# Kernel optimization log

Measured on AMD Instinct MI355X. Metric: run time of the kernel, lower is better.

The kernel has to match this reference:

```python
import jax, jax.numpy as jnp
import numpy as np
from jax import lax

NUM_GROUP = 512
GROUP_SIZE = 32


def fps(xyz, npoint):
    """Farthest point sampling. xyz: [B, N, 3] -> centers [B, npoint, 3]."""
    B, N, _ = xyz.shape
    big = jnp.asarray(1e10, xyz.dtype)

    def body(carry, _):
        min_d, farthest = carry  # [B, N], [B]
        centroid = jnp.take_along_axis(xyz, farthest[:, None, None], axis=1)  # [B,1,3]
        d = jnp.sum((xyz - centroid) ** 2, axis=-1)  # [B, N]
        min_d = jnp.minimum(min_d, d)
        nxt = jnp.argmax(min_d, axis=-1).astype(jnp.int32)
        return (min_d, nxt), farthest

    init = (jnp.full((B, N), big, xyz.dtype), jnp.zeros((B,), jnp.int32))
    _, idxs = lax.scan(body, init, None, length=npoint)  # [npoint, B]
    idxs = idxs.T  # [B, npoint]
    return jnp.take_along_axis(xyz, idxs[..., None], axis=1)  # [B, npoint, 3]


def knn_idx(xyz, center, k):
    """xyz [B,N,3], center [B,G,3] -> idx [B,G,k] of k nearest (squared L2)."""
    # [B, G, N] squared distances
    d2 = jnp.sum((center[:, :, None, :] - xyz[:, None, :, :]) ** 2, axis=-1)
    _, idx = lax.top_k(-d2, k)  # smallest distances
    return idx


def setup_inputs() -> dict:
    key = jax.random.key(0)
    xyz = jax.random.normal(key, (32, 3, 8192), dtype=jnp.float32)
    return {"xyz": xyz}


def reference(xyz):
    # xyz: [B, 3, N] -> [B, N, 3]
    pts = jnp.transpose(xyz, (0, 2, 1))[:, :, :3]
    B, N, _ = pts.shape
    center = fps(pts, NUM_GROUP)                  # [B, G, 3]
    idx = knn_idx(pts, center, GROUP_SIZE)        # [B, G, k]
    flat_idx = idx.reshape(B, NUM_GROUP * GROUP_SIZE)
    neighborhood = jnp.take_along_axis(pts, flat_idx[..., None], axis=1)
    neighborhood = neighborhood.reshape(B, NUM_GROUP, GROUP_SIZE, 3)
    neighborhood = neighborhood - center[:, :, None, :]
    return neighborhood, center
```

## Files before the change

### kernel.cpp

```cpp
#include <hip/hip_runtime.h>

typedef unsigned long long u64;
typedef unsigned int u32;
typedef float v2f __attribute__((ext_vector_type(2)));

#define BATCH 32
#define NPTS  8192
#define NGRP  512
#define KNN_K 32

#define FPS_T 256
#define FPS_W (FPS_T / 64)
#define PPAIR (NPTS / FPS_T / 2)

#define KNN_WPB 8
#define KNN_T   (KNN_WPB * 64)
#define QCAP    128

#define NCH     (NPTS / 64)
#define GC      16
#define NCELL   (GC * GC * GC)
#define QB      512
#define CBT     256
#define WSF     (4 * NPTS + NCH * 6)

__device__ __forceinline__ float sq3(float dx, float dy, float dz) {
    return __fadd_rn(__fadd_rn(__fmul_rn(dx, dx), __fmul_rn(dy, dy)), __fmul_rn(dz, dz));
}

__device__ __forceinline__ u64 packdi(float d, int n) {
    return ((u64)__float_as_uint(d) << 32) | (u32)n;
}

__device__ __forceinline__ u64 umin64(u64 a, u64 b) { return a < b ? a : b; }
__device__ __forceinline__ u64 umax64(u64 a, u64 b) { return a > b ? a : b; }

__device__ __forceinline__ u64 shfl_xor_u64(u64 v, int m) {
    int lo = __shfl_xor((int)(u32)v, m, 64);
    int hi = __shfl_xor((int)(u32)(v >> 32), m, 64);
    return ((u64)(u32)hi << 32) | (u32)lo;
}

__device__ __forceinline__ u64 shfl_u64(u64 v, int src) {
    int lo = __shfl((int)(u32)v, src, 64);
    int hi = __shfl((int)(u32)(v >> 32), src, 64);
    return ((u64)(u32)hi << 32) | (u32)lo;
}

template <int CTRL>
__device__ __forceinline__ u64 dpp_max_step(u64 k) {
    u32 plo = (u32)__builtin_amdgcn_update_dpp(0, (int)(u32)k, CTRL, 0xF, 0xF, true);
    u32 phi = (u32)__builtin_amdgcn_update_dpp(0, (int)(u32)(k >> 32), CTRL, 0xF, 0xF, true);
    u64 p = ((u64)phi << 32) | plo;
    return k > p ? k : p;
}
__device__ __forceinline__ u64 dpp_wave_max(u64 k) {
    k = dpp_max_step<0x111>(k);
    k = dpp_max_step<0x112>(k);
    k = dpp_max_step<0x114>(k);
    k = dpp_max_step<0x118>(k);
    k = dpp_max_step<0x142>(k);
    k = dpp_max_step<0x143>(k);
    return k;
}

__device__ __forceinline__ u64 lane_sort64(u64 v, int lane) {
#pragma unroll
    for (int k = 2; k <= 64; k <<= 1) {
#pragma unroll
        for (int j = k >> 1; j > 0; j >>= 1) {
            u64 p = shfl_xor_u64(v, j);
            bool keepmin = (((lane & k) == 0) == ((lane & j) == 0));
            u64 mn = umin64(v, p), mx = umax64(v, p);
            v = keepmin ? mn : mx;
        }
    }
    return v;
}

__device__ __forceinline__ u64 lane_merge64(u64 m, u64 c, int lane) {
    u64 cr = shfl_xor_u64(c, 63);
    u64 z = umin64(m, cr);
#pragma unroll
    for (int dd = 32; dd > 0; dd >>= 1) {
        u64 p = shfl_xor_u64(z, dd);
        u64 mn = umin64(z, p), mx = umax64(z, p);
        z = (lane & dd) ? mx : mn;
    }
    return z;
}

__device__ __forceinline__ void knn_step(u64& m, u64& tau, int& cnt, u64* sbuf,
                                         float x, float y, float z,
                                         float cx, float cy, float cz,
                                         int n, int lane) {
    float d = sq3(__fsub_rn(x, cx), __fsub_rn(y, cy), __fsub_rn(z, cz));
    u64 kk = packdi(d, n);
    bool cand = kk < tau;
    u64 mask = __ballot(cand);
    if (mask) {
        u32 below = __builtin_amdgcn_mbcnt_hi(
            (u32)(mask >> 32), __builtin_amdgcn_mbcnt_lo((u32)mask, 0));
        if (cand) sbuf[cnt + below] = kk;
        cnt += (int)__popcll(mask);
        if (cnt >= 64) {
            u64 c = sbuf[lane];
            c = lane_sort64(c, lane);
            m = lane_merge64(m, c, lane);
            tau = shfl_u64(m, 31);
            int rem = cnt - 64;
            if (lane < rem) sbuf[lane] = sbuf[64 + lane];
            cnt = rem;
        }
    }
}

__device__ __forceinline__ int qbin(float v) {
    int c = (int)((v + 4.0f) * 64.0f);
    c = c < 0 ? 0 : c;
    return c > (QB - 1) ? (QB - 1) : c;
}
__device__ __forceinline__ u32 part3_4(u32 v) {
    return (v & 1u) | ((v & 2u) << 2) | ((v & 4u) << 4) | ((v & 8u) << 6);
}

struct FpsLds {
    float sx[NPTS]; float sy[NPTS]; float sz[NPTS];
    u64 s_key[2][FPS_W];
    float s_out[NGRP * 3];
};
struct BldLds {
    u32 hist[NCELL];
    u32 hq[3][QB];
    float sxl[NPTS]; float syl[NPTS]; float szl[NPTS];
    u32 wtot[3][CBT / 64];
};

__global__ __launch_bounds__(CBT) void fps_build_kernel(const float* __restrict__ in,
                                                        float* __restrict__ ws,
                                                        float* __restrict__ centers) {
#pragma clang fp contract(off)
    __shared__ alignas(16) char smem[sizeof(BldLds)];

    const int t = threadIdx.x;
    const int lane = t & 63;
    const int w = t >> 6;

    if (blockIdx.x < BATCH) {
        FpsLds& S = *reinterpret_cast<FpsLds*>(smem);
        const int b = blockIdx.x;
        const float* xp = in + (size_t)b * 3 * NPTS;
        const float* yp = xp + NPTS;
        const float* zp = xp + 2 * NPTS;

        v2f xr[PPAIR], yr[PPAIR], zr[PPAIR], md[PPAIR];
#pragma unroll
        for (int i = 0; i < PPAIR; ++i) {
            int n = i * (2 * FPS_T) + 2 * t;
            xr[i] = *(const v2f*)(xp + n);
            yr[i] = *(const v2f*)(yp + n);
            zr[i] = *(const v2f*)(zp + n);
            *(v2f*)(S.sx + n) = xr[i];
            *(v2f*)(S.sy + n) = yr[i];
            *(v2f*)(S.sz + n) = zr[i];
            md[i] = (v2f){1e10f, 1e10f};
        }
        __syncthreads();

        int cur = 0;
        for (int r = 0; r < NGRP; ++r) {
            const float cx = S.sx[cur], cy = S.sy[cur], cz = S.sz[cur];
            if (t == 0) {
                S.s_out[r * 3 + 0] = cx;
                S.s_out[r * 3 + 1] = cy;
                S.s_out[r * 3 + 2] = cz;
            }

            float bd0 = -1.0f, bd1 = -1.0f;
            int   bi0 = 0,     bi1 = 0;
#pragma unroll
            for (int i = 0; i < PPAIR; ++i) {
                v2f dx = xr[i] - cx;
                v2f dy = yr[i] - cy;
                v2f dz = zr[i] - cz;
                v2f dd = dx * dx + dy * dy + dz * dz;
                md[i] = __builtin_elementwise_min(md[i], dd);
                int n = i * (2 * FPS_T) + 2 * t;
                if (md[i].x > bd0) { bd0 = md[i].x; bi0 = n; }
                if (md[i].y > bd1) { bd1 = md[i].y; bi1 = n + 1; }
            }
            u64 k0 = ((u64)__float_as_uint(bd0) << 32) | (u32)(~(u32)bi0);
            u64 k1 = ((u64)__float_as_uint(bd1) << 32) | (u32)(~(u32)bi1);
            u64 k = dpp_wave_max(umax64(k0, k1));
            if ((t & 63) == 63) S.s_key[r & 1][w] = k;
            __syncthreads();
            u64 m = umax64(umax64(S.s_key[r & 1][0], S.s_key[r & 1][1]),
                           umax64(S.s_key[r & 1][2], S.s_key[r & 1][3]));
            cur = (int)(~(u32)m);
        }

        __syncthreads();
        float* cdst = centers + (size_t)b * NGRP * 3;
        for (int i = t; i < NGRP * 3; i += FPS_T) cdst[i] = S.s_out[i];
        return;
    }

    BldLds& S = *reinterpret_cast<BldLds*>(smem);
    const int b = blockIdx.x - BATCH;
    const float* xp = in + (size_t)b * 3 * NPTS;
    const float* yp = xp + NPTS;
    const float* zp = xp + 2 * NPTS;
    float* wsb = ws + (size_t)b * WSF;
    float* ws_sx = wsb;
    float* ws_sy = wsb + NPTS;
    float* ws_sz = wsb + 2 * NPTS;
    u32*   ws_si = (u32*)(wsb + 3 * NPTS);
    float* ws_ab = wsb + 4 * NPTS;

    for (int i = t; i < NCELL; i += CBT) S.hist[i] = 0;
    for (int i = t; i < 3 * QB; i += CBT) (&S.hq[0][0])[i] = 0;
    __syncthreads();

    for (int i = t; i < NPTS; i += CBT) {
        atomicAdd(&S.hq[0][qbin(xp[i])], 1u);
        atomicAdd(&S.hq[1][qbin(yp[i])], 1u);
        atomicAdd(&S.hq[2][qbin(zp[i])], 1u);
    }
    __syncthreads();

    {
        u32 va0 = S.hq[0][2 * t], vb0 = S.hq[0][2 * t + 1];
        u32 va1 = S.hq[1][2 * t], vb1 = S.hq[1][2 * t + 1];
        u32 va2 = S.hq[2][2 * t], vb2 = S.hq[2][2 * t + 1];
        u32 s0 = va0 + vb0, s1 = va1 + vb1, s2 = va2 + vb2;
        u32 x0 = s0, x1 = s1, x2 = s2;
#pragma unroll
        for (int d = 1; d < 64; d <<= 1) {
            u32 y0 = __shfl_up(x0, d, 64), y1 = __shfl_up(x1, d, 64), y2 = __shfl_up(x2, d, 64);
            if (lane >= d) { x0 += y0; x1 += y1; x2 += y2; }
        }
        if (lane == 63) { S.wtot[0][w] = x0; S.wtot[1][w] = x1; S.wtot[2][w] = x2; }
        __syncthreads();
        u32 b0 = 0, b1 = 0, b2 = 0;
        for (int j = 0; j < w; ++j) { b0 += S.wtot[0][j]; b1 += S.wtot[1][j]; b2 += S.wtot[2][j]; }
        u32 e0 = b0 + x0 - s0, e1 = b1 + x1 - s1, e2 = b2 + x2 - s2;
        S.hq[0][2 * t] = e0 >> 9;  S.hq[0][2 * t + 1] = (e0 + va0) >> 9;
        S.hq[1][2 * t] = e1 >> 9;  S.hq[1][2 * t + 1] = (e1 + va1) >> 9;
        S.hq[2][2 * t] = e2 >> 9;  S.hq[2][2 * t + 1] = (e2 + va2) >> 9;
    }
    __syncthreads();

    for (int i = t; i < NPTS; i += CBT) {
        int pc = (int)(part3_4(S.hq[0][qbin(xp[i])]) |
                       (part3_4(S.hq[1][qbin(yp[i])]) << 1) |
                       (part3_4(S.hq[2][qbin(zp[i])]) << 2));
        atomicAdd(&S.hist[pc], 1u);
    }
    __syncthreads();

    {
        u32 h[NCELL / CBT];
        u32 lsum = 0;
#pragma unroll
        for (int j = 0; j < NCELL / CBT; ++j) { h[j] = S.hist[t * (NCELL / CBT) + j]; lsum += h[j]; }
        u32 x = lsum;
#pragma unroll
        for (int d = 1; d < 64; d <<= 1) {
            u32 y = __shfl_up(x, d, 64);
            if (lane >= d) x += y;
        }
        if (lane == 63) S.wtot[0][w] = x;
        __syncthreads();
        u32 base = 0;
        for (int j = 0; j < w; ++j) base += S.wtot[0][j];
        u32 run = base + x - lsum;
#pragma unroll
        for (int j = 0; j < NCELL / CBT; ++j) {
            u32 c = h[j];
            S.hist[t * (NCELL / CBT) + j] = run;
            run += c;
        }
    }
    __syncthreads();

    for (int i = t; i < NPTS; i += CBT) {
        float X = xp[i], Y = yp[i], Z = zp[i];
        int pc = (int)(part3_4(S.hq[0][qbin(X)]) |
                       (part3_4(S.hq[1][qbin(Y)]) << 1) |
                       (part3_4(S.hq[2][qbin(Z)]) << 2));
        u32 pos = atomicAdd(&S.hist[pc], 1u);
        S.sxl[pos] = X; S.syl[pos] = Y; S.szl[pos] = Z;
        ws_si[pos] = (u32)i;
    }
    __syncthreads();

    for (int i = t; i < NPTS; i += CBT) {
        ws_sx[i] = S.sxl[i]; ws_sy[i] = S.syl[i]; ws_sz[i] = S.szl[i];
    }
    for (int q = w; q < NCH; q += CBT / 64) {
        int p = q * 64 + lane;
        float X = S.sxl[p], Y = S.syl[p], Z = S.szl[p];
        float xlo = X, xhi = X, ylo = Y, yhi = Y, zlo = Z, zhi = Z;
#pragma unroll
        for (int d = 1; d < 64; d <<= 1) {
            xlo = fminf(xlo, __shfl_xor(xlo, d, 64)); xhi = fmaxf(xhi, __shfl_xor(xhi, d, 64));
            ylo = fminf(ylo, __shfl_xor(ylo, d, 64)); yhi = fmaxf(yhi, __shfl_xor(yhi, d, 64));
            zlo = fminf(zlo, __shfl_xor(zlo, d, 64)); zhi = fmaxf(zhi, __shfl_xor(zhi, d, 64));
        }
        if (lane == 0) {
            float* a = ws_ab + q * 6;
            a[0] = xlo; a[1] = xhi; a[2] = ylo; a[3] = yhi; a[4] = zlo; a[5] = zhi;
        }
    }
}

__global__ __launch_bounds__(KNN_T) void knn_kernel(const float* __restrict__ in,
                                                    const float* __restrict__ centers,
                                                    const float* __restrict__ ws,
                                                    float* __restrict__ out) {
    __shared__ float s_ab[NCH * 6];
    __shared__ u64 sbuf[KNN_WPB][QCAP];

    const int wave = threadIdx.x >> 6;
    const int lane = threadIdx.x & 63;
    const int cid  = blockIdx.x * KNN_WPB + wave;
    const int b    = cid >> 9;

    const float* xp = in + (size_t)b * 3 * NPTS;
    const float* yp = xp + NPTS;
    const float* zp = xp + 2 * NPTS;
    const float* wsb = ws + (size_t)b * WSF;
    const float* sxs = wsb;
    const float* sys = wsb + NPTS;
    const float* szs = wsb + 2 * NPTS;
    const u32*   sidx = (const u32*)(wsb + 3 * NPTS);
    const float* ab = wsb + 4 * NPTS;

    for (int i = threadIdx.x; i < NCH * 6; i += KNN_T) s_ab[i] = ab[i];
    __syncthreads();

    const float cx = centers[cid * 3 + 0];
    const float cy = centers[cid * 3 + 1];
    const float cz = centers[cid * 3 + 2];

    u64 k0, k1;
    {
        const float* a0 = &s_ab[lane * 6];
        float dx = fmaxf(fmaxf(__fsub_rn(a0[0], cx), __fsub_rn(cx, a0[1])), 0.0f);
        float dy = fmaxf(fmaxf(__fsub_rn(a0[2], cy), __fsub_rn(cy, a0[3])), 0.0f);
        float dz = fmaxf(fmaxf(__fsub_rn(a0[4], cz), __fsub_rn(cz, a0[5])), 0.0f);
        k0 = ((u64)__float_as_uint(dx * dx + dy * dy + dz * dz) << 32) | (u32)lane;
        const float* a1 = &s_ab[(lane + 64) * 6];
        dx = fmaxf(fmaxf(__fsub_rn(a1[0], cx), __fsub_rn(cx, a1[1])), 0.0f);
        dy = fmaxf(fmaxf(__fsub_rn(a1[2], cy), __fsub_rn(cy, a1[3])), 0.0f);
        dz = fmaxf(fmaxf(__fsub_rn(a1[4], cz), __fsub_rn(cz, a1[5])), 0.0f);
        k1 = ((u64)__float_as_uint(dx * dx + dy * dy + dz * dz) << 32) | (u32)(lane + 64);
    }

    u64 m, tau;
    int cnt = 0;

    {
        u64 inv = dpp_wave_max(~umin64(k0, k1));
        u64 got = ~shfl_u64(inv, 63);
        int c = (int)(u32)got;
        int p = c * 64 + lane;
        float X = sxs[p], Y = sys[p], Z = szs[p];
        int n = (int)sidx[p];
        m = lane_sort64(packdi(sq3(__fsub_rn(X, cx), __fsub_rn(Y, cy), __fsub_rn(Z, cz)), n),
                        lane);
        tau = shfl_u64(m, 31);
        if (lane == (c & 63)) { if (c < 64) k0 = ~0ull; else k1 = ~0ull; }
    }

    for (int it = 1; it < NCH; ++it) {
        u64 inv = dpp_wave_max(~umin64(k0, k1));
        u64 got = ~shfl_u64(inv, 63);
        float lb = __uint_as_float((u32)(got >> 32));
        float tau_d = __uint_as_float((u32)(tau >> 32));
        if (lb * 0.999f > tau_d) break;
        int c = (int)(u32)got;
        int p = c * 64 + lane;
        float X = sxs[p], Y = sys[p], Z = szs[p];
        int n = (int)sidx[p];
        knn_step(m, tau, cnt, sbuf[wave], X, Y, Z, cx, cy, cz, n, lane);
        if (lane == (c & 63)) { if (c < 64) k0 = ~0ull; else k1 = ~0ull; }
    }

    while (cnt > 0) {
        int take = cnt < 64 ? cnt : 64;
        u64 v = sbuf[wave][lane];
        u64 c = (lane < take) ? v : ~0ull;
        c = lane_sort64(c, lane);
        m = lane_merge64(m, c, lane);
        int rem = cnt - take;
        if (lane < rem) sbuf[wave][lane] = sbuf[wave][64 + lane];
        cnt = rem;
    }

    if (lane < KNN_K) {
        int n = (int)(u32)m;
        size_t o = (size_t)cid * (KNN_K * 3) + (size_t)lane * 3;
        out[o + 0] = __fsub_rn(xp[n], cx);
        out[o + 1] = __fsub_rn(yp[n], cy);
        out[o + 2] = __fsub_rn(zp[n], cz);
    }
}

__global__ __launch_bounds__(FPS_T) void fps_kernel(const float* __restrict__ in,
                                                    float* __restrict__ centers) {
#pragma clang fp contract(off)
    __shared__ float sx[NPTS];
    __shared__ float sy[NPTS];
    __shared__ float sz[NPTS];
    __shared__ u64 s_key[2][FPS_W];
    __shared__ float s_out[NGRP * 3];

    const int b = blockIdx.x;
    const int t = threadIdx.x;
    const int w = t >> 6;
    const float* xp = in + (size_t)b * 3 * NPTS;
    const float* yp = xp + NPTS;
    const float* zp = xp + 2 * NPTS;

    v2f xr[PPAIR], yr[PPAIR], zr[PPAIR], md[PPAIR];
#pragma unroll
    for (int i = 0; i < PPAIR; ++i) {
        int n = i * (2 * FPS_T) + 2 * t;
        xr[i] = *(const v2f*)(xp + n);
        yr[i] = *(const v2f*)(yp + n);
        zr[i] = *(const v2f*)(zp + n);
        *(v2f*)(sx + n) = xr[i];
        *(v2f*)(sy + n) = yr[i];
        *(v2f*)(sz + n) = zr[i];
        md[i] = (v2f){1e10f, 1e10f};
    }
    __syncthreads();

    int cur = 0;
    for (int r = 0; r < NGRP; ++r) {
        const float cx = sx[cur], cy = sy[cur], cz = sz[cur];
        if (t == 0) {
            s_out[r * 3 + 0] = cx;
            s_out[r * 3 + 1] = cy;
            s_out[r * 3 + 2] = cz;
        }
        float bd0 = -1.0f, bd1 = -1.0f;
        int   bi0 = 0,     bi1 = 0;
#pragma unroll
        for (int i = 0; i < PPAIR; ++i) {
            v2f dx = xr[i] - cx;
            v2f dy = yr[i] - cy;
            v2f dz = zr[i] - cz;
            v2f dd = dx * dx + dy * dy + dz * dz;
            md[i] = __builtin_elementwise_min(md[i], dd);
            int n = i * (2 * FPS_T) + 2 * t;
            if (md[i].x > bd0) { bd0 = md[i].x; bi0 = n; }
            if (md[i].y > bd1) { bd1 = md[i].y; bi1 = n + 1; }
        }
        u64 k0 = ((u64)__float_as_uint(bd0) << 32) | (u32)(~(u32)bi0);
        u64 k1 = ((u64)__float_as_uint(bd1) << 32) | (u32)(~(u32)bi1);
        u64 k = dpp_wave_max(umax64(k0, k1));
        if ((t & 63) == 63) s_key[r & 1][w] = k;
        __syncthreads();
        u64 m = umax64(umax64(s_key[r & 1][0], s_key[r & 1][1]),
                       umax64(s_key[r & 1][2], s_key[r & 1][3]));
        cur = (int)(~(u32)m);
    }

    __syncthreads();
    float* cdst = centers + (size_t)b * NGRP * 3;
    for (int i = t; i < NGRP * 3; i += FPS_T) cdst[i] = s_out[i];
}

#define KNN_WPB_FB 4
__global__ __launch_bounds__(KNN_WPB_FB * 64) void knn_fallback(
    const float* __restrict__ in, const float* __restrict__ centers,
    float* __restrict__ out) {
    __shared__ u64 sbuf[KNN_WPB_FB][QCAP];

    const int wave = threadIdx.x >> 6;
    const int lane = threadIdx.x & 63;
    const int cid  = blockIdx.x * KNN_WPB_FB + wave;
    const int b    = cid >> 9;

    const float* xp = in + (size_t)b * 3 * NPTS;
    const float* yp = xp + NPTS;
    const float* zp = xp + 2 * NPTS;

    const float cx = centers[cid * 3 + 0];
    const float cy = centers[cid * 3 + 1];
    const float cz = centers[cid * 3 + 2];

    float x = xp[lane], y = yp[lane], z = zp[lane];
    u64 m = packdi(sq3(__fsub_rn(x, cx), __fsub_rn(y, cy), __fsub_rn(z, cz)), lane);
    m = lane_sort64(m, lane);
    u64 tau = shfl_u64(m, 31);
    int cnt = 0;

    int j = 1;
#pragma unroll 1
    for (; j + 3 < NPTS / 64; j += 4) {
        int n0 = j * 64 + lane, n1 = n0 + 64, n2 = n0 + 128, n3 = n0 + 192;
        float x0 = xp[n0], y0 = yp[n0], z0 = zp[n0];
        float x1 = xp[n1], y1 = yp[n1], z1 = zp[n1];
        float x2 = xp[n2], y2 = yp[n2], z2 = zp[n2];
        float x3 = xp[n3], y3 = yp[n3], z3 = zp[n3];
        knn_step(m, tau, cnt, sbuf[wave], x0, y0, z0, cx, cy, cz, n0, lane);
        knn_step(m, tau, cnt, sbuf[wave], x1, y1, z1, cx, cy, cz, n1, lane);
        knn_step(m, tau, cnt, sbuf[wave], x2, y2, z2, cx, cy, cz, n2, lane);
        knn_step(m, tau, cnt, sbuf[wave], x3, y3, z3, cx, cy, cz, n3, lane);
    }
    for (; j < NPTS / 64; ++j) {
        int n = j * 64 + lane;
        knn_step(m, tau, cnt, sbuf[wave], xp[n], yp[n], zp[n], cx, cy, cz, n, lane);
    }
    while (cnt > 0) {
        int take = cnt < 64 ? cnt : 64;
        u64 v = sbuf[wave][lane];
        u64 c = (lane < take) ? v : ~0ull;
        c = lane_sort64(c, lane);
        m = lane_merge64(m, c, lane);
        int rem = cnt - take;
        if (lane < rem) sbuf[wave][lane] = sbuf[wave][64 + lane];
        cnt = rem;
    }
    if (lane < KNN_K) {
        int n = (int)(u32)m;
        size_t o = (size_t)cid * (KNN_K * 3) + (size_t)lane * 3;
        out[o + 0] = __fsub_rn(xp[n], cx);
        out[o + 1] = __fsub_rn(yp[n], cy);
        out[o + 2] = __fsub_rn(zp[n], cz);
    }
}

extern "C" void kernel_launch(void* const* d_in, const int* in_sizes, int n_in,
                              void* d_out, int out_size, void* d_ws, size_t ws_size,
                              hipStream_t stream) {
    const float* in  = (const float*)d_in[0];
    float* out       = (float*)d_out;
    float* centers   = out + (size_t)BATCH * NGRP * KNN_K * 3;

    const size_t need = (size_t)BATCH * WSF * sizeof(float);

    if (d_ws != nullptr && ws_size >= need) {
        fps_build_kernel<<<2 * BATCH, CBT, 0, stream>>>(in, (float*)d_ws, centers);
        knn_kernel<<<(BATCH * NGRP) / KNN_WPB, KNN_T, 0, stream>>>(
            in, centers, (const float*)d_ws, out);
    } else {
        fps_kernel<<<BATCH, FPS_T, 0, stream>>>(in, centers);
        knn_fallback<<<(BATCH * NGRP) / KNN_WPB_FB, KNN_WPB_FB * 64, 0, stream>>>(
            in, centers, out);
    }
}
```

Measured before the change: 530.9 us.

## Presort chunk bounds in KNN, prefetch next chunk, pack points as float4

The build kernel now scatters sorted points straight to global memory as packed float4 records (x, y, z, index) instead of staging them in LDS and writing four separate arrays. The KNN kernel sorts all 128 chunk lower bounds once with a bitonic merge, rather than running a wave-wide max reduction on every iteration. It then walks chunks in sorted order and software-prefetches the next chunk's float4 while the current one is processed. This cuts per-iteration reduction cost and load latency. In exchange it adds an upfront full sort, a wasted prefetch at loop exit, and scattered global writes in the build phase.

```diff
diff --git a/kernel.cpp b/kernel.cpp
--- a/kernel.cpp
+++ b/kernel.cpp
@@ -132,7 +132,6 @@
 struct BldLds {
     u32 hist[NCELL];
     u32 hq[3][QB];
-    float sxl[NPTS]; float syl[NPTS]; float szl[NPTS];
     u32 wtot[3][CBT / 64];
 };
 
@@ -140,7 +139,7 @@
                                                         float* __restrict__ ws,
                                                         float* __restrict__ centers) {
 #pragma clang fp contract(off)
-    __shared__ alignas(16) char smem[sizeof(BldLds)];
+    __shared__ alignas(16) char smem[sizeof(FpsLds)];
 
     const int t = threadIdx.x;
     const int lane = t & 63;
@@ -211,11 +210,8 @@
     const float* yp = xp + NPTS;
     const float* zp = xp + 2 * NPTS;
     float* wsb = ws + (size_t)b * WSF;
-    float* ws_sx = wsb;
-    float* ws_sy = wsb + NPTS;
-    float* ws_sz = wsb + 2 * NPTS;
-    u32*   ws_si = (u32*)(wsb + 3 * NPTS);
-    float* ws_ab = wsb + 4 * NPTS;
+    float4* ws_p4 = (float4*)wsb;
+    float*  ws_ab = wsb + 4 * NPTS;
 
     for (int i = t; i < NCELL; i += CBT) S.hist[i] = 0;
     for (int i = t; i < 3 * QB; i += CBT) (&S.hq[0][0])[i] = 0;
@@ -289,18 +285,13 @@
                        (part3_4(S.hq[1][qbin(Y)]) << 1) |
                        (part3_4(S.hq[2][qbin(Z)]) << 2));
         u32 pos = atomicAdd(&S.hist[pc], 1u);
-        S.sxl[pos] = X; S.syl[pos] = Y; S.szl[pos] = Z;
-        ws_si[pos] = (u32)i;
-    }
-    __syncthreads();
-
-    for (int i = t; i < NPTS; i += CBT) {
-        ws_sx[i] = S.sxl[i]; ws_sy[i] = S.syl[i]; ws_sz[i] = S.szl[i];
-    }
+        ws_p4[pos] = make_float4(X, Y, Z, __uint_as_float((u32)i));
+    }
+    __syncthreads();
+
     for (int q = w; q < NCH; q += CBT / 64) {
-        int p = q * 64 + lane;
-        float X = S.sxl[p], Y = S.syl[p], Z = S.szl[p];
-        float xlo = X, xhi = X, ylo = Y, yhi = Y, zlo = Z, zhi = Z;
+        float4 P = ws_p4[q * 64 + lane];
+        float xlo = P.x, xhi = P.x, ylo = P.y, yhi = P.y, zlo = P.z, zhi = P.z;
 #pragma unroll
         for (int d = 1; d < 64; d <<= 1) {
             xlo = fminf(xlo, __shfl_xor(xlo, d, 64)); xhi = fmaxf(xhi, __shfl_xor(xhi, d, 64));
@@ -330,10 +321,7 @@
     const float* yp = xp + NPTS;
     const float* zp = xp + 2 * NPTS;
     const float* wsb = ws + (size_t)b * WSF;
-    const float* sxs = wsb;
-    const float* sys = wsb + NPTS;
-    const float* szs = wsb + 2 * NPTS;
-    const u32*   sidx = (const u32*)(wsb + 3 * NPTS);
+    const float4* p4 = (const float4*)wsb;
     const float* ab = wsb + 4 * NPTS;
 
     for (int i = threadIdx.x; i < NCH * 6; i += KNN_T) s_ab[i] = ab[i];
@@ -357,34 +345,51 @@
         k1 = ((u64)__float_as_uint(dx * dx + dy * dy + dz * dz) << 32) | (u32)(lane + 64);
     }
 
+    u64 lo, hi;
+    {
+        k0 = lane_sort64(k0, lane);
+        k1 = lane_sort64(k1, lane);
+        u64 c1r = shfl_xor_u64(k1, 63);
+        lo = umin64(k0, c1r);
+        hi = umax64(k0, c1r);
+#pragma unroll
+        for (int dd = 32; dd > 0; dd >>= 1) {
+            u64 pl = shfl_xor_u64(lo, dd);
+            u64 ph = shfl_xor_u64(hi, dd);
+            u64 lmn = umin64(lo, pl), lmx = umax64(lo, pl);
+            u64 hmn = umin64(hi, ph), hmx = umax64(hi, ph);
+            lo = (lane & dd) ? lmx : lmn;
+            hi = (lane & dd) ? hmx : hmn;
+        }
+    }
+
     u64 m, tau;
     int cnt = 0;
 
+    float4 cur;
     {
-        u64 inv = dpp_wave_max(~umin64(k0, k1));
-        u64 got = ~shfl_u64(inv, 63);
-        int c = (int)(u32)got;
-        int p = c * 64 + lane;
-        float X = sxs[p], Y = sys[p], Z = szs[p];
-        int n = (int)sidx[p];
-        m = lane_sort64(packdi(sq3(__fsub_rn(X, cx), __fsub_rn(Y, cy), __fsub_rn(Z, cz)), n),
+        u64 key0 = shfl_u64(lo, 0);
+        float4 c0 = p4[((int)(u32)key0) * 64 + lane];
+        u64 key1 = shfl_u64(lo, 1);
+        cur = p4[((int)(u32)key1) * 64 + lane];
+        m = lane_sort64(packdi(sq3(__fsub_rn(c0.x, cx), __fsub_rn(c0.y, cy),
+                                   __fsub_rn(c0.z, cz)),
+                               (int)__float_as_uint(c0.w)),
                         lane);
         tau = shfl_u64(m, 31);
-        if (lane == (c & 63)) { if (c < 64) k0 = ~0ull; else k1 = ~0ull; }
-    }
-
-    for (int it = 1; it < NCH; ++it) {
-        u64 inv = dpp_wave_max(~umin64(k0, k1));
-        u64 got = ~shfl_u64(inv, 63);
-        float lb = __uint_as_float((u32)(got >> 32));
+    }
+
+    for (int r = 1; r < NCH; ++r) {
+        int rn = (r + 1 < NCH) ? r + 1 : NCH - 1;
+        u64 kn = (rn < 64) ? shfl_u64(lo, rn) : shfl_u64(hi, rn - 64);
+        float4 nxt = p4[((int)(u32)kn) * 64 + lane];
+        u64 key = (r < 64) ? shfl_u64(lo, r) : shfl_u64(hi, r - 64);
+        float lb = __uint_as_float((u32)(key >> 32));
         float tau_d = __uint_as_float((u32)(tau >> 32));
         if (lb * 0.999f > tau_d) break;
-        int c = (int)(u32)got;
-        int p = c * 64 + lane;
-        float X = sxs[p], Y = sys[p], Z = szs[p];
-        int n = (int)sidx[p];
-        knn_step(m, tau, cnt, sbuf[wave], X, Y, Z, cx, cy, cz, n, lane);
-        if (lane == (c & 63)) { if (c < 64) k0 = ~0ull; else k1 = ~0ull; }
+        knn_step(m, tau, cnt, sbuf[wave], cur.x, cur.y, cur.z, cx, cy, cz,
+                 (int)__float_as_uint(cur.w), lane);
+        cur = nxt;
     }
 
     while (cnt > 0) {
```

Measured after the change: 539.7 us. Within noise of the previous version (+1.7%).

## Fuse FPS, grid build and KNN into one kernel with flag-based streaming

Applied to the files above, without the earlier changes.

Merges the FPS/build kernel and the KNN kernel into a single persistent launch. FPS blocks publish centers in chunks of 16 with release flags, and KNN blocks (6 per batch, 4 waves each) spin on those flags and the build-done flag, so neighbor search overlaps the sequential FPS loop. This hides KNN behind FPS latency and removes the second launch. In exchange it relies on all 256 blocks being co-resident to avoid deadlock, adds a memset and spin-wait traffic, and leaves fewer waves for KNN.

```diff
diff --git a/kernel.cpp b/kernel.cpp
--- a/kernel.cpp
+++ b/kernel.cpp
@@ -13,13 +13,12 @@
 #define FPS_W (FPS_T / 64)
 #define PPAIR (NPTS / FPS_T / 2)
 
-#define KNN_WPB 8
-#define KNN_T   (KNN_WPB * 64)
 #define QCAP    128
+#define NKB     6
+#define NWAVE_B (NKB * 4)
 
 #define NCH     (NPTS / 64)
-#define GC      16
-#define NCELL   (GC * GC * GC)
+#define NCELL   (16 * 16 * 16)
 #define QB      512
 #define CBT     256
 #define WSF     (4 * NPTS + NCH * 6)
@@ -135,10 +134,17 @@
     float sxl[NPTS]; float syl[NPTS]; float szl[NPTS];
     u32 wtot[3][CBT / 64];
 };
-
-__global__ __launch_bounds__(CBT) void fps_build_kernel(const float* __restrict__ in,
-                                                        float* __restrict__ ws,
-                                                        float* __restrict__ centers) {
+struct KnnLds {
+    float s_ab[NCH * 6];
+    u64 sbuf[CBT / 64][QCAP];
+};
+
+__global__ __launch_bounds__(CBT) void fused_kernel(const float* __restrict__ in,
+                                                    float* __restrict__ ws,
+                                                    u32* __restrict__ flags,
+                                                    u32* __restrict__ build_done,
+                                                    float* __restrict__ centers,
+                                                    float* __restrict__ out) {
 #pragma clang fp contract(off)
     __shared__ alignas(16) char smem[sizeof(BldLds)];
 
@@ -152,6 +158,7 @@
         const float* xp = in + (size_t)b * 3 * NPTS;
         const float* yp = xp + NPTS;
         const float* zp = xp + 2 * NPTS;
+        u32* cball = (u32*)(centers + (size_t)b * NGRP * 3);
 
         v2f xr[PPAIR], yr[PPAIR], zr[PPAIR], md[PPAIR];
 #pragma unroll
@@ -197,134 +204,141 @@
             u64 m = umax64(umax64(S.s_key[r & 1][0], S.s_key[r & 1][1]),
                            umax64(S.s_key[r & 1][2], S.s_key[r & 1][3]));
             cur = (int)(~(u32)m);
-        }
-
-        __syncthreads();
-        float* cdst = centers + (size_t)b * NGRP * 3;
-        for (int i = t; i < NGRP * 3; i += FPS_T) cdst[i] = S.s_out[i];
+
+            if (t == 0 && (r & 15) == 15) {
+                const int base = (r - 15) * 3;
+#pragma unroll 4
+                for (int j = 0; j < 48; ++j)
+                    __hip_atomic_store(cball + base + j,
+                                       __float_as_uint(S.s_out[base + j]),
+                                       __ATOMIC_RELAXED, __HIP_MEMORY_SCOPE_AGENT);
+                __hip_atomic_store(&flags[b], (u32)(r + 1),
+                                   __ATOMIC_RELEASE, __HIP_MEMORY_SCOPE_AGENT);
+            }
+        }
         return;
     }
 
-    BldLds& S = *reinterpret_cast<BldLds*>(smem);
-    const int b = blockIdx.x - BATCH;
-    const float* xp = in + (size_t)b * 3 * NPTS;
-    const float* yp = xp + NPTS;
-    const float* zp = xp + 2 * NPTS;
-    float* wsb = ws + (size_t)b * WSF;
-    float* ws_sx = wsb;
-    float* ws_sy = wsb + NPTS;
-    float* ws_sz = wsb + 2 * NPTS;
-    u32*   ws_si = (u32*)(wsb + 3 * NPTS);
-    float* ws_ab = wsb + 4 * NPTS;
-
-    for (int i = t; i < NCELL; i += CBT) S.hist[i] = 0;
-    for (int i = t; i < 3 * QB; i += CBT) (&S.hq[0][0])[i] = 0;
-    __syncthreads();
-
-    for (int i = t; i < NPTS; i += CBT) {
-        atomicAdd(&S.hq[0][qbin(xp[i])], 1u);
-        atomicAdd(&S.hq[1][qbin(yp[i])], 1u);
-        atomicAdd(&S.hq[2][qbin(zp[i])], 1u);
-    }
-    __syncthreads();
-
-    {
-        u32 va0 = S.hq[0][2 * t], vb0 = S.hq[0][2 * t + 1];
-        u32 va1 = S.hq[1][2 * t], vb1 = S.hq[1][2 * t + 1];
-        u32 va2 = S.hq[2][2 * t], vb2 = S.hq[2][2 * t + 1];
-        u32 s0 = va0 + vb0, s1 = va1 + vb1, s2 = va2 + vb2;
-        u32 x0 = s0, x1 = s1, x2 = s2;
-#pragma unroll
-        for (int d = 1; d < 64; d <<= 1) {
-            u32 y0 = __shfl_up(x0, d, 64), y1 = __shfl_up(x1, d, 64), y2 = __shfl_up(x2, d, 64);
-            if (lane >= d) { x0 += y0; x1 += y1; x2 += y2; }
-        }
-        if (lane == 63) { S.wtot[0][w] = x0; S.wtot[1][w] = x1; S.wtot[2][w] = x2; }
-        __syncthreads();
-        u32 b0 = 0, b1 = 0, b2 = 0;
-        for (int j = 0; j < w; ++j) { b0 += S.wtot[0][j]; b1 += S.wtot[1][j]; b2 += S.wtot[2][j]; }
-        u32 e0 = b0 + x0 - s0, e1 = b1 + x1 - s1, e2 = b2 + x2 - s2;
-        S.hq[0][2 * t] = e0 >> 9;  S.hq[0][2 * t + 1] = (e0 + va0) >> 9;
-        S.hq[1][2 * t] = e1 >> 9;  S.hq[1][2 * t + 1] = (e1 + va1) >> 9;
-        S.hq[2][2 * t] = e2 >> 9;  S.hq[2][2 * t + 1] = (e2 + va2) >> 9;
-    }
-    __syncthreads();
-
-    for (int i = t; i < NPTS; i += CBT) {
-        int pc = (int)(part3_4(S.hq[0][qbin(xp[i])]) |
-                       (part3_4(S.hq[1][qbin(yp[i])]) << 1) |
-                       (part3_4(S.hq[2][qbin(zp[i])]) << 2));
-        atomicAdd(&S.hist[pc], 1u);
-    }
-    __syncthreads();
-
-    {
-        u32 h[NCELL / CBT];
-        u32 lsum = 0;
-#pragma unroll
-        for (int j = 0; j < NCELL / CBT; ++j) { h[j] = S.hist[t * (NCELL / CBT) + j]; lsum += h[j]; }
-        u32 x = lsum;
-#pragma unroll
-        for (int d = 1; d < 64; d <<= 1) {
-            u32 y = __shfl_up(x, d, 64);
-            if (lane >= d) x += y;
-        }
-        if (lane == 63) S.wtot[0][w] = x;
-        __syncthreads();
-        u32 base = 0;
-        for (int j = 0; j < w; ++j) base += S.wtot[0][j];
-        u32 run = base + x - lsum;
-#pragma unroll
-        for (int j = 0; j < NCELL / CBT; ++j) {
-            u32 c = h[j];
-            S.hist[t * (NCELL / CBT) + j] = run;
-            run += c;
-        }
-    }
-    __syncthreads();
-
-    for (int i = t; i < NPTS; i += CBT) {
-        float X = xp[i], Y = yp[i], Z = zp[i];
-        int pc = (int)(part3_4(S.hq[0][qbin(X)]) |
-                       (part3_4(S.hq[1][qbin(Y)]) << 1) |
-                       (part3_4(S.hq[2][qbin(Z)]) << 2));
-        u32 pos = atomicAdd(&S.hist[pc], 1u);
-        S.sxl[pos] = X; S.syl[pos] = Y; S.szl[pos] = Z;
-        ws_si[pos] = (u32)i;
-    }
-    __syncthreads();
-
-    for (int i = t; i < NPTS; i += CBT) {
-        ws_sx[i] = S.sxl[i]; ws_sy[i] = S.syl[i]; ws_sz[i] = S.szl[i];
-    }
-    for (int q = w; q < NCH; q += CBT / 64) {
-        int p = q * 64 + lane;
-        float X = S.sxl[p], Y = S.syl[p], Z = S.szl[p];
-        float xlo = X, xhi = X, ylo = Y, yhi = Y, zlo = Z, zhi = Z;
-#pragma unroll
-        for (int d = 1; d < 64; d <<= 1) {
-            xlo = fminf(xlo, __shfl_xor(xlo, d, 64)); xhi = fmaxf(xhi, __shfl_xor(xhi, d, 64));
-            ylo = fminf(ylo, __shfl_xor(ylo, d, 64)); yhi = fmaxf(yhi, __shfl_xor(yhi, d, 64));
-            zlo = fminf(zlo, __shfl_xor(zlo, d, 64)); zhi = fmaxf(zhi, __shfl_xor(zhi, d, 64));
-        }
-        if (lane == 0) {
-            float* a = ws_ab + q * 6;
-            a[0] = xlo; a[1] = xhi; a[2] = ylo; a[3] = yhi; a[4] = zlo; a[5] = zhi;
-        }
-    }
-}
-
-__global__ __launch_bounds__(KNN_T) void knn_kernel(const float* __restrict__ in,
-                                                    const float* __restrict__ centers,
-                                                    const float* __restrict__ ws,
-                                                    float* __restrict__ out) {
-    __shared__ float s_ab[NCH * 6];
-    __shared__ u64 sbuf[KNN_WPB][QCAP];
-
-    const int wave = threadIdx.x >> 6;
-    const int lane = threadIdx.x & 63;
-    const int cid  = blockIdx.x * KNN_WPB + wave;
-    const int b    = cid >> 9;
+    if (blockIdx.x < 2 * BATCH) {
+        BldLds& S = *reinterpret_cast<BldLds*>(smem);
+        const int b = blockIdx.x - BATCH;
+        const float* xp = in + (size_t)b * 3 * NPTS;
+        const float* yp = xp + NPTS;
+        const float* zp = xp + 2 * NPTS;
+        float* wsb = ws + (size_t)b * WSF;
+        float* ws_sx = wsb;
+        float* ws_sy = wsb + NPTS;
+        float* ws_sz = wsb + 2 * NPTS;
+        u32*   ws_si = (u32*)(wsb + 3 * NPTS);
+        float* ws_ab = wsb + 4 * NPTS;
+
+        for (int i = t; i < NCELL; i += CBT) S.hist[i] = 0;
+        for (int i = t; i < 3 * QB; i += CBT) (&S.hq[0][0])[i] = 0;
+        __syncthreads();
+
+        for (int i = t; i < NPTS; i += CBT) {
+            atomicAdd(&S.hq[0][qbin(xp[i])], 1u);
+            atomicAdd(&S.hq[1][qbin(yp[i])], 1u);
+            atomicAdd(&S.hq[2][qbin(zp[i])], 1u);
+        }
+        __syncthreads();
+
+        {
+            u32 va0 = S.hq[0][2 * t], vb0 = S.hq[0][2 * t + 1];
+            u32 va1 = S.hq[1][2 * t], vb1 = S.hq[1][2 * t + 1];
+            u32 va2 = S.hq[2][2 * t], vb2 = S.hq[2][2 * t + 1];
+            u32 s0 = va0 + vb0, s1 = va1 + vb1, s2 = va2 + vb2;
+            u32 x0 = s0, x1 = s1, x2 = s2;
+#pragma unroll
+            for (int d = 1; d < 64; d <<= 1) {
+                u32 y0 = __shfl_up(x0, d, 64), y1 = __shfl_up(x1, d, 64), y2 = __shfl_up(x2, d, 64);
+                if (lane >= d) { x0 += y0; x1 += y1; x2 += y2; }
+            }
+            if (lane == 63) { S.wtot[0][w] = x0; S.wtot[1][w] = x1; S.wtot[2][w] = x2; }
+            __syncthreads();
+            u32 b0 = 0, b1 = 0, b2 = 0;
+            for (int j = 0; j < w; ++j) { b0 += S.wtot[0][j]; b1 += S.wtot[1][j]; b2 += S.wtot[2][j]; }
+            u32 e0 = b0 + x0 - s0, e1 = b1 + x1 - s1, e2 = b2 + x2 - s2;
+            S.hq[0][2 * t] = e0 >> 9;  S.hq[0][2 * t + 1] = (e0 + va0) >> 9;
+            S.hq[1][2 * t] = e1 >> 9;  S.hq[1][2 * t + 1] = (e1 + va1) >> 9;
+            S.hq[2][2 * t] = e2 >> 9;  S.hq[2][2 * t + 1] = (e2 + va2) >> 9;
+        }
+        __syncthreads();
+
+        for (int i = t; i < NPTS; i += CBT) {
+            int pc = (int)(part3_4(S.hq[0][qbin(xp[i])]) |
+                           (part3_4(S.hq[1][qbin(yp[i])]) << 1) |
+                           (part3_4(S.hq[2][qbin(zp[i])]) << 2));
+            atomicAdd(&S.hist[pc], 1u);
+        }
+        __syncthreads();
+
+        {
+            u32 h[NCELL / CBT];
+            u32 lsum = 0;
+#pragma unroll
+            for (int j = 0; j < NCELL / CBT; ++j) { h[j] = S.hist[t * (NCELL / CBT) + j]; lsum += h[j]; }
+            u32 x = lsum;
+#pragma unroll
+            for (int d = 1; d < 64; d <<= 1) {
+                u32 y = __shfl_up(x, d, 64);
+                if (lane >= d) x += y;
+            }
+            if (lane == 63) S.wtot[0][w] = x;
+            __syncthreads();
+            u32 base = 0;
+            for (int j = 0; j < w; ++j) base += S.wtot[0][j];
+            u32 run = base + x - lsum;
+#pragma unroll
+            for (int j = 0; j < NCELL / CBT; ++j) {
+                u32 c = h[j];
+                S.hist[t * (NCELL / CBT) + j] = run;
+                run += c;
+            }
+        }
+        __syncthreads();
+
+        for (int i = t; i < NPTS; i += CBT) {
+            float X = xp[i], Y = yp[i], Z = zp[i];
+            int pc = (int)(part3_4(S.hq[0][qbin(X)]) |
+                           (part3_4(S.hq[1][qbin(Y)]) << 1) |
+                           (part3_4(S.hq[2][qbin(Z)]) << 2));
+            u32 pos = atomicAdd(&S.hist[pc], 1u);
+            S.sxl[pos] = X; S.syl[pos] = Y; S.szl[pos] = Z;
+            ws_si[pos] = (u32)i;
+        }
+        __syncthreads();
+
+        for (int i = t; i < NPTS; i += CBT) {
+            ws_sx[i] = S.sxl[i]; ws_sy[i] = S.syl[i]; ws_sz[i] = S.szl[i];
+        }
+        for (int q = w; q < NCH; q += CBT / 64) {
+            int p = q * 64 + lane;
+            float X = S.sxl[p], Y = S.syl[p], Z = S.szl[p];
+            float xlo = X, xhi = X, ylo = Y, yhi = Y, zlo = Z, zhi = Z;
+#pragma unroll
+            for (int d = 1; d < 64; d <<= 1) {
+                xlo = fminf(xlo, __shfl_xor(xlo, d, 64)); xhi = fmaxf(xhi, __shfl_xor(xhi, d, 64));
+                ylo = fminf(ylo, __shfl_xor(ylo, d, 64)); yhi = fmaxf(yhi, __shfl_xor(yhi, d, 64));
+                zlo = fminf(zlo, __shfl_xor(zlo, d, 64)); zhi = fmaxf(zhi, __shfl_xor(zhi, d, 64));
+            }
+            if (lane == 0) {
+                float* a = ws_ab + q * 6;
+                a[0] = xlo; a[1] = xhi; a[2] = ylo; a[3] = yhi; a[4] = zlo; a[5] = zhi;
+            }
+        }
+        __syncthreads();
+        if (t == 0)
+            __hip_atomic_store(&build_done[b], 1u,
+                               __ATOMIC_RELEASE, __HIP_MEMORY_SCOPE_AGENT);
+        return;
+    }
+
+    KnnLds& S = *reinterpret_cast<KnnLds*>(smem);
+    const int kb   = blockIdx.x - 2 * BATCH;
+    const int b    = kb / NKB;
+    const int sub  = kb % NKB;
+    const int wave = w;
 
     const float* xp = in + (size_t)b * 3 * NPTS;
     const float* yp = xp + NPTS;
@@ -335,75 +349,99 @@
     const float* szs = wsb + 2 * NPTS;
     const u32*   sidx = (const u32*)(wsb + 3 * NPTS);
     const float* ab = wsb + 4 * NPTS;
-
-    for (int i = threadIdx.x; i < NCH * 6; i += KNN_T) s_ab[i] = ab[i];
+    const u32* cball = (const u32*)(centers + (size_t)b * NGRP * 3);
+
+    if (t == 0) {
+        while (__hip_atomic_load(&build_done[b], __ATOMIC_ACQUIRE,
+                                 __HIP_MEMORY_SCOPE_AGENT) == 0)
+            __builtin_amdgcn_s_sleep(16);
+    }
     __syncthreads();
-
-    const float cx = centers[cid * 3 + 0];
-    const float cy = centers[cid * 3 + 1];
-    const float cz = centers[cid * 3 + 2];
-
-    u64 k0, k1;
-    {
-        const float* a0 = &s_ab[lane * 6];
-        float dx = fmaxf(fmaxf(__fsub_rn(a0[0], cx), __fsub_rn(cx, a0[1])), 0.0f);
-        float dy = fmaxf(fmaxf(__fsub_rn(a0[2], cy), __fsub_rn(cy, a0[3])), 0.0f);
-        float dz = fmaxf(fmaxf(__fsub_rn(a0[4], cz), __fsub_rn(cz, a0[5])), 0.0f);
-        k0 = ((u64)__float_as_uint(dx * dx + dy * dy + dz * dz) << 32) | (u32)lane;
-        const float* a1 = &s_ab[(lane + 64) * 6];
-        dx = fmaxf(fmaxf(__fsub_rn(a1[0], cx), __fsub_rn(cx, a1[1])), 0.0f);
-        dy = fmaxf(fmaxf(__fsub_rn(a1[2], cy), __fsub_rn(cy, a1[3])), 0.0f);
-        dz = fmaxf(fmaxf(__fsub_rn(a1[4], cz), __fsub_rn(cz, a1[5])), 0.0f);
-        k1 = ((u64)__float_as_uint(dx * dx + dy * dy + dz * dz) << 32) | (u32)(lane + 64);
-    }
-
-    u64 m, tau;
-    int cnt = 0;
-
-    {
-        u64 inv = dpp_wave_max(~umin64(k0, k1));
-        u64 got = ~shfl_u64(inv, 63);
-        int c = (int)(u32)got;
-        int p = c * 64 + lane;
-        float X = sxs[p], Y = sys[p], Z = szs[p];
-        int n = (int)sidx[p];
-        m = lane_sort64(packdi(sq3(__fsub_rn(X, cx), __fsub_rn(Y, cy), __fsub_rn(Z, cz)), n),
-                        lane);
-        tau = shfl_u64(m, 31);
-        if (lane == (c & 63)) { if (c < 64) k0 = ~0ull; else k1 = ~0ull; }
-    }
-
-    for (int it = 1; it < NCH; ++it) {
-        u64 inv = dpp_wave_max(~umin64(k0, k1));
-        u64 got = ~shfl_u64(inv, 63);
-        float lb = __uint_as_float((u32)(got >> 32));
-        float tau_d = __uint_as_float((u32)(tau >> 32));
-        if (lb * 0.999f > tau_d) break;
-        int c = (int)(u32)got;
-        int p = c * 64 + lane;
-        float X = sxs[p], Y = sys[p], Z = szs[p];
-        int n = (int)sidx[p];
-        knn_step(m, tau, cnt, sbuf[wave], X, Y, Z, cx, cy, cz, n, lane);
-        if (lane == (c & 63)) { if (c < 64) k0 = ~0ull; else k1 = ~0ull; }
-    }
-
-    while (cnt > 0) {
-        int take = cnt < 64 ? cnt : 64;
-        u64 v = sbuf[wave][lane];
-        u64 c = (lane < take) ? v : ~0ull;
-        c = lane_sort64(c, lane);
-        m = lane_merge64(m, c, lane);
-        int rem = cnt - take;
-        if (lane < rem) sbuf[wave][lane] = sbuf[wave][64 + lane];
-        cnt = rem;
-    }
-
-    if (lane < KNN_K) {
-        int n = (int)(u32)m;
-        size_t o = (size_t)cid * (KNN_K * 3) + (size_t)lane * 3;
-        out[o + 0] = __fsub_rn(xp[n], cx);
-        out[o + 1] = __fsub_rn(yp[n], cy);
-        out[o + 2] = __fsub_rn(zp[n], cz);
+    for (int i = t; i < NCH * 6; i += CBT) S.s_ab[i] = ab[i];
+    __syncthreads();
+
+    const int wg = sub * 4 + wave;
+    for (int g = wg; g < NGRP; g += NWAVE_B) {
+        float cxl = 0.f, cyl = 0.f, czl = 0.f;
+        if (lane == 0) {
+            while (__hip_atomic_load(&flags[b], __ATOMIC_ACQUIRE,
+                                     __HIP_MEMORY_SCOPE_AGENT) <= (u32)g)
+                __builtin_amdgcn_s_sleep(8);
+            const u32* cs = cball + (size_t)g * 3;
+            cxl = __uint_as_float(__hip_atomic_load(cs + 0, __ATOMIC_RELAXED,
+                                                    __HIP_MEMORY_SCOPE_AGENT));
+            cyl = __uint_as_float(__hip_atomic_load(cs + 1, __ATOMIC_RELAXED,
+                                                    __HIP_MEMORY_SCOPE_AGENT));
+            czl = __uint_as_float(__hip_atomic_load(cs + 2, __ATOMIC_RELAXED,
+                                                    __HIP_MEMORY_SCOPE_AGENT));
+        }
+        const float cx = __shfl(cxl, 0, 64);
+        const float cy = __shfl(cyl, 0, 64);
+        const float cz = __shfl(czl, 0, 64);
+        const int cid = (b << 9) + g;
+
+        u64 k0, k1;
+        {
+            const float* a0 = &S.s_ab[lane * 6];
+            float dx = fmaxf(fmaxf(__fsub_rn(a0[0], cx), __fsub_rn(cx, a0[1])), 0.0f);
+            float dy = fmaxf(fmaxf(__fsub_rn(a0[2], cy), __fsub_rn(cy, a0[3])), 0.0f);
+            float dz = fmaxf(fmaxf(__fsub_rn(a0[4], cz), __fsub_rn(cz, a0[5])), 0.0f);
+            k0 = ((u64)__float_as_uint(dx * dx + dy * dy + dz * dz) << 32) | (u32)lane;
+            const float* a1 = &S.s_ab[(lane + 64) * 6];
+            dx = fmaxf(fmaxf(__fsub_rn(a1[0], cx), __fsub_rn(cx, a1[1])), 0.0f);
+            dy = fmaxf(fmaxf(__fsub_rn(a1[2], cy), __fsub_rn(cy, a1[3])), 0.0f);
+            dz = fmaxf(fmaxf(__fsub_rn(a1[4], cz), __fsub_rn(cz, a1[5])), 0.0f);
+            k1 = ((u64)__float_as_uint(dx * dx + dy * dy + dz * dz) << 32) | (u32)(lane + 64);
+        }
+
+        u64 m, tau;
+        int cnt = 0;
+
+        {
+            u64 inv = dpp_wave_max(~umin64(k0, k1));
+            u64 got = ~shfl_u64(inv, 63);
+            int c = (int)(u32)got;
+            int p = c * 64 + lane;
+            float X = sxs[p], Y = sys[p], Z = szs[p];
+            int n = (int)sidx[p];
+            m = lane_sort64(packdi(sq3(__fsub_rn(X, cx), __fsub_rn(Y, cy),
+                                       __fsub_rn(Z, cz)), n), lane);
+            tau = shfl_u64(m, 31);
+            if (lane == (c & 63)) { if (c < 64) k0 = ~0ull; else k1 = ~0ull; }
+        }
+
+        for (int it = 1; it < NCH; ++it) {
+            u64 inv = dpp_wave_max(~umin64(k0, k1));
+            u64 got = ~shfl_u64(inv, 63);
+            float lb = __uint_as_float((u32)(got >> 32));
+            float tau_d = __uint_as_float((u32)(tau >> 32));
+            if (lb * 0.999f > tau_d) break;
+            int c = (int)(u32)got;
+            int p = c * 64 + lane;
+            float X = sxs[p], Y = sys[p], Z = szs[p];
+            int n = (int)sidx[p];
+            knn_step(m, tau, cnt, S.sbuf[wave], X, Y, Z, cx, cy, cz, n, lane);
+            if (lane == (c & 63)) { if (c < 64) k0 = ~0ull; else k1 = ~0ull; }
+        }
+
+        while (cnt > 0) {
+            int take = cnt < 64 ? cnt : 64;
+            u64 v = S.sbuf[wave][lane];
+            u64 c = (lane < take) ? v : ~0ull;
+            c = lane_sort64(c, lane);
+            m = lane_merge64(m, c, lane);
+            int rem = cnt - take;
+            if (lane < rem) S.sbuf[wave][lane] = S.sbuf[wave][64 + lane];
+            cnt = rem;
+        }
+
+        if (lane < KNN_K) {
+            int n = (int)(u32)m;
+            size_t o = (size_t)cid * (KNN_K * 3) + (size_t)lane * 3;
+            out[o + 0] = __fsub_rn(xp[n], cx);
+            out[o + 1] = __fsub_rn(yp[n], cy);
+            out[o + 2] = __fsub_rn(zp[n], cz);
+        }
     }
 }
 
@@ -541,12 +579,15 @@
     float* out       = (float*)d_out;
     float* centers   = out + (size_t)BATCH * NGRP * KNN_K * 3;
 
-    const size_t need = (size_t)BATCH * WSF * sizeof(float);
+    const size_t need = ((size_t)BATCH * WSF + 2 * BATCH) * sizeof(float);
 
     if (d_ws != nullptr && ws_size >= need) {
-        fps_build_kernel<<<2 * BATCH, CBT, 0, stream>>>(in, (float*)d_ws, centers);
-        knn_kernel<<<(BATCH * NGRP) / KNN_WPB, KNN_T, 0, stream>>>(
-            in, centers, (const float*)d_ws, out);
+        float* ws = (float*)d_ws;
+        u32* flags = (u32*)(ws + (size_t)BATCH * WSF);
+        u32* build_done = flags + BATCH;
+        hipMemsetAsync(flags, 0, 2 * BATCH * sizeof(u32), stream);
+        fused_kernel<<<8 * BATCH, CBT, 0, stream>>>(in, ws, flags, build_done,
+                                                    centers, out);
     } else {
         fps_kernel<<<BATCH, FPS_T, 0, stream>>>(in, centers);
         knn_fallback<<<(BATCH * NGRP) / KNN_WPB_FB, KNN_WPB_FB * 64, 0, stream>>>(
```

Measured after the change: 673.8 us. 26.9% more time.
